# Performance work log

Hardware: AMD Instinct MI355X
Metric: run time of the kernel (lower is better)

The kernel has to match this reference:

```python
import jax, jax.numpy as jnp
import numpy as np

HIP_L, HIP_R = 11, 12          # hip joint indices along V
K_LIST = (2, 3, 4, 5)          # soft-selector kNN MoE k values
TAU = 0.35                     # tau_center for ball softmax
EPS = 1e-6


def _sym_norm(A):
    # D^{-1/2} A D^{-1/2} without materializing diag matrices
    d = A.sum(-1)
    dis = jax.lax.rsqrt(d + EPS)
    return dis[..., :, None] * A * dis[..., None, :]


def _knn_adj(pos, k):
    # pos: (N, M, 3) -> 0/1 kNN adjacency (+I self loop, diag ends up 2 as in torch ref)
    M = pos.shape[1]
    diff = pos[:, :, None, :] - pos[:, None, :, :]
    d = jnp.sqrt(jnp.sum(diff * diff, axis=-1))  # (N, M, M) euclidean cdist
    idx = jax.lax.top_k(-d, k)[1]                # (N, M, k) k smallest distances (incl. self)
    A = jax.nn.one_hot(idx, M, dtype=pos.dtype).sum(2)  # scatter 1.0 at kNN columns
    return A + jnp.eye(M, dtype=pos.dtype)


def setup_inputs() -> dict:
    key = jax.random.key(0)
    k1, k2 = jax.random.split(key)
    N, C, T, V, M = 64, 8, 300, 17, 12
    x = jax.random.normal(k1, (N, C, T, V, M), jnp.float32)
    alpha_logits = jax.random.normal(k2, (len(K_LIST),), jnp.float32) * 0.1
    lambda_fuse = jnp.array([0.1], jnp.float32)
    tag_gate = jnp.array([1.0], jnp.float32)
    return {"x": x, "alpha_logits": alpha_logits,
            "lambda_fuse": lambda_fuse, "tag_gate": tag_gate}


def reference(x, alpha_logits, lambda_fuse, tag_gate):
    N, C, T, V, M = x.shape
    # hip-root position averaged over time: (N, M, 3)
    root3 = 0.5 * (x[:, 0:3, :, HIP_L, :] + x[:, 0:3, :, HIP_R, :])  # (N,3,T,M)
    pos = root3.mean(2).transpose(0, 2, 1)                           # (N,M,3)

    # kNN mixture-of-graphs, sym-normalized, detached (detach_adj=True)
    A_knn_stack = jnp.stack([_sym_norm(_knn_adj(pos, k)) for k in K_LIST], 1)  # (N,K,M,M)
    A_knn_stack = jax.lax.stop_gradient(A_knn_stack)
    alpha = jax.nn.softmax(alpha_logits)          # global selector, temp=1
    A_knn = jnp.einsum('k,nkij->nij', alpha, A_knn_stack)

    # soft ball-star graph
    s = x[:, 3].mean((1, 2))                      # (N,M) ball score
    p = jax.nn.softmax(s / TAU, axis=1)
    A_ball = p[:, :, None] + p[:, None, :] + jnp.eye(M, dtype=x.dtype)
    A_ball = jax.lax.stop_gradient(_sym_norm(A_ball))

    # adaptive ball weight from confidence of p (NOT detached)
    w = jnp.clip((jnp.max(p, 1, keepdims=True) - 1.0 / M) / (1.0 - 1.0 / M + EPS), 0.0, 1.0)
    A = w[:, :, None] * A_ball + (1.0 - w[:, :, None]) * A_knn  # (N,M,M)

    # message passing across persons on hip-root features, fused back residually
    root = 0.5 * (x[:, :, :, HIP_L, :] + x[:, :, :, HIP_R, :])  # (N,C,T,M)
    agg = jnp.einsum('nuv,nctv->nctu', A, root)                 # (N,C,T,M)
    g = jnp.tanh(tag_gate[0])  # ramp=1 (ramp_epochs=0), gate_max=1
    return x + g * lambda_fuse[0] * (agg - root)[:, :, :, None, :]
```

## Files before the change

kernel.cpp:

```cpp
#include <hip/hip_runtime.h>
#include <math.h>

#define N_ 64
#define C_ 8
#define T_ 300
#define V_ 17
#define M_ 12
#define EPSF 1e-6f
#define TAUF 0.35f


__global__ __launch_bounds__(256) void k_reduce(const float* __restrict__ x,
                                                float* __restrict__ ws_pos,
                                                float* __restrict__ ws_s) {
    const int n = blockIdx.x;
    const int tid = threadIdx.x;
    __shared__ float pos_acc[36];
    __shared__ float s_acc[12];
    if (tid < 36) pos_acc[tid] = 0.f;
    if (tid < 12) s_acc[tid] = 0.f;
    __syncthreads();

    {
        float a[3][3];
        #pragma unroll
        for (int d = 0; d < 3; ++d)
            #pragma unroll
            for (int ph = 0; ph < 3; ++ph) a[d][ph] = 0.f;
        for (int e = tid; e < 3600; e += 768) {
            #pragma unroll
            for (int ph = 0; ph < 3; ++ph) {
                int ee = e + ph * 256;
                if (ee < 3600) {
                    int t = ee / 12, m = ee % 12;
                    #pragma unroll
                    for (int d = 0; d < 3; ++d) {
                        const float* xb = x + ((size_t)(n * C_ + d) * T_ + t) * (V_ * M_);
                        a[d][ph] += xb[132 + m] + xb[144 + m];
                    }
                }
            }
        }
        int m0 = tid % 12;
        #pragma unroll
        for (int ph = 0; ph < 3; ++ph) {
            int m = (m0 + 4 * ph) % 12;
            #pragma unroll
            for (int d = 0; d < 3; ++d) atomicAdd(&pos_acc[d * 12 + m], a[d][ph]);
        }
    }

    {
        float a0 = 0.f, a1 = 0.f, a2 = 0.f;
        const float* xs = x + (size_t)(n * C_ + 3) * T_ * V_ * M_;
        for (int e = tid; e < 61200; e += 768) {
            a0 += xs[e];
            if (e + 256 < 61200) a1 += xs[e + 256];
            if (e + 512 < 61200) a2 += xs[e + 512];
        }
        int m0 = tid % 12;
        atomicAdd(&s_acc[m0], a0);
        atomicAdd(&s_acc[(m0 + 4) % 12], a1);
        atomicAdd(&s_acc[(m0 + 8) % 12], a2);
    }
    __syncthreads();
    if (tid < 36) ws_pos[n * 36 + tid] = pos_acc[tid] * (0.5f / (float)T_);
    if (tid < 12) ws_s[n * 12 + tid] = s_acc[tid] * (1.f / (float)(T_ * V_));
}

__global__ __launch_bounds__(64) void k_adj(const float* __restrict__ ws_pos,
                                            const float* __restrict__ ws_s,
                                            const float* __restrict__ alpha_logits,
                                            float* __restrict__ ws_A) {
    const int n = blockIdx.x;
    const int tid = threadIdx.x;
    __shared__ float posx[12], posy[12], posz[12];
    __shared__ float dist[144];
    __shared__ int ord[60];
    __shared__ float p_s[12];
    __shared__ float alpha_s[4];
    __shared__ float w_s;

    if (tid < 12) {
        posx[tid] = ws_pos[n * 36 + 0 * 12 + tid];
        posy[tid] = ws_pos[n * 36 + 1 * 12 + tid];
        posz[tid] = ws_pos[n * 36 + 2 * 12 + tid];
    }
    if (tid == 0) {
        float l0 = alpha_logits[0], l1 = alpha_logits[1], l2 = alpha_logits[2], l3 = alpha_logits[3];
        float mx = fmaxf(fmaxf(l0, l1), fmaxf(l2, l3));
        float e0 = expf(l0 - mx), e1 = expf(l1 - mx), e2 = expf(l2 - mx), e3 = expf(l3 - mx);
        float s = e0 + e1 + e2 + e3;
        alpha_s[0] = e0 / s; alpha_s[1] = e1 / s; alpha_s[2] = e2 / s; alpha_s[3] = e3 / s;
    }
    if (tid == 1) {
        float sv[12];
        float mx = -1e30f;
        #pragma unroll
        for (int m = 0; m < 12; ++m) { sv[m] = ws_s[n * 12 + m] * (1.f / TAUF); mx = fmaxf(mx, sv[m]); }
        float sum = 0.f;
        #pragma unroll
        for (int m = 0; m < 12; ++m) { sv[m] = expf(sv[m] - mx); sum += sv[m]; }
        float maxp = 0.f;
        #pragma unroll
        for (int m = 0; m < 12; ++m) { sv[m] = sv[m] / sum; p_s[m] = sv[m]; maxp = fmaxf(maxp, sv[m]); }
        float w = (maxp - 1.f / 12.f) / (1.f - 1.f / 12.f + EPSF);
        w_s = fminf(fmaxf(w, 0.f), 1.f);
    }
    __syncthreads();

    for (int e = tid; e < 144; e += 64) {
        int i = e / 12, j = e % 12;
        float dx = posx[i] - posx[j], dy = posy[i] - posy[j], dz = posz[i] - posz[j];
        dist[e] = sqrtf(dx * dx + dy * dy + dz * dz);
    }
    __syncthreads();

    if (tid < 12) {
        int i = tid, mask = 0;
        #pragma unroll
        for (int r = 0; r < 5; ++r) {
            float bd = 1e30f; int bj = -1;
            #pragma unroll
            for (int j = 0; j < 12; ++j) {
                if (!((mask >> j) & 1)) {
                    float dd = dist[i * 12 + j];
                    if (dd < bd) { bd = dd; bj = j; }
                }
            }
            ord[i * 5 + r] = bj; mask |= (1 << bj);
        }
    }
    __syncthreads();

    float w = w_s;
    for (int e = tid; e < 144; e += 64) {
        int i = e / 12, j = e % 12;
        int rank = 5;
        #pragma unroll
        for (int r = 4; r >= 0; --r) if (ord[i * 5 + r] == j) rank = r;
        float diag = (i == j) ? 1.f : 0.f;
        float aknn = 0.f;
        #pragma unroll
        for (int kk = 0; kk < 4; ++kk) {
            int K = kk + 2;
            float val = ((rank < K) ? 1.f : 0.f) + diag;
            aknn += alpha_s[kk] * val / ((float)(K + 1) + EPSF);
        }
        float pi = p_s[i], pj = p_s[j];
        float di = 12.f * pi + 2.f, dj = 12.f * pj + 2.f;
        float ab = (pi + pj + diag) * rsqrtf(di + EPSF) * rsqrtf(dj + EPSF);
        ws_A[n * 144 + e] = w * ab + (1.f - w) * aknn;
    }
}

#define RT 30
__global__ __launch_bounds__(256) void k_main(const float* __restrict__ x,
                                              const float* __restrict__ ws_A,
                                              const float* __restrict__ lambda_fuse,
                                              const float* __restrict__ tag_gate,
                                              float* __restrict__ out) {
    const int n = blockIdx.y;
    const int r0 = blockIdx.x * RT;
    const int tid = threadIdx.x;
    __shared__ float Ash[144];
    __shared__ float root_sh[RT * 12];
    __shared__ float delta_sh[RT * 12];

    if (tid < 144) Ash[tid] = ws_A[n * 144 + tid];
    float scale = tanhf(tag_gate[0]) * lambda_fuse[0];

    const float* xn = x + (size_t)n * 2400 * 204;
    float* on = out + (size_t)n * 2400 * 204;

    for (int e = tid; e < RT * 12; e += 256) {
        int r = e / 12, v = e % 12;
        const float* row = xn + (size_t)(r0 + r) * 204;
        root_sh[e] = 0.5f * (row[132 + v] + row[144 + v]);
    }
    __syncthreads();
    for (int e = tid; e < RT * 12; e += 256) {
        int r = e / 12, u = e % 12;
        float acc = 0.f;
        #pragma unroll
        for (int v = 0; v < 12; ++v) acc += Ash[u * 12 + v] * root_sh[r * 12 + v];
        delta_sh[e] = scale * (acc - root_sh[e]);
    }
    __syncthreads();

    const float4* x4 = (const float4*)(xn + (size_t)r0 * 204);
    float4* o4 = (float4*)(on + (size_t)r0 * 204);
    for (int f = tid; f < RT * 51; f += 256) {
        int r = f / 51, j = f % 51;
        int m0 = (4 * j) % 12;
        float4 v = x4[(size_t)r * 51 + j];
        const float* d = &delta_sh[r * 12 + m0];
        v.x += d[0]; v.y += d[1]; v.z += d[2]; v.w += d[3];
        o4[(size_t)r * 51 + j] = v;
    }
}

extern "C" void kernel_launch(void* const* d_in, const int* in_sizes, int n_in,
                              void* d_out, int out_size, void* d_ws, size_t ws_size,
                              hipStream_t stream) {
    const float* x = (const float*)d_in[0];
    const float* alpha_logits = (const float*)d_in[1];
    const float* lambda_fuse = (const float*)d_in[2];
    const float* tag_gate = (const float*)d_in[3];
    float* out = (float*)d_out;

    float* ws = (float*)d_ws;
    float* ws_pos = ws;
    float* ws_s = ws + 64 * 36;
    float* ws_A = ws + 64 * 36 + 64 * 12;

    k_reduce<<<dim3(N_), dim3(256), 0, stream>>>(x, ws_pos, ws_s);
    k_adj<<<dim3(N_), dim3(64), 0, stream>>>(ws_pos, ws_s, alpha_logits, ws_A);
    k_main<<<dim3(2400 / RT, N_), dim3(256), 0, stream>>>(x, ws_A, lambda_fuse, tag_gate, out);
}
```

Before: 306.9 us.

## Split reduction kernel across time chunks with global atomics

The per-sample reduction kernel is split along the time axis into 10 chunks, so 640 blocks run instead of 64. Partial sums are combined with global atomicAdd into a workspace that is zeroed by a memset, and the scaling moves into the adjacency kernel. The hip-joint gather is also rewritten as a flat loop with per-element shared atomics. This targets low occupancy in the reduction, in exchange for an extra memset launch, global atomics, and non-deterministic summation order.

```diff
diff --git a/kernel.cpp b/kernel.cpp
--- a/kernel.cpp
+++ b/kernel.cpp
@@ -10,10 +10,14 @@
 #define TAUF 0.35f
 
 
+#define TSPLIT 10
+#define TCH (T_ / TSPLIT)
+
 __global__ __launch_bounds__(256) void k_reduce(const float* __restrict__ x,
                                                 float* __restrict__ ws_pos,
                                                 float* __restrict__ ws_s) {
     const int n = blockIdx.x;
+    const int t0 = blockIdx.y * TCH;
     const int tid = threadIdx.x;
     __shared__ float pos_acc[36];
     __shared__ float s_acc[12];
@@ -22,50 +26,30 @@
     __syncthreads();
 
     {
-        float a[3][3];
-        #pragma unroll
-        for (int d = 0; d < 3; ++d)
-            #pragma unroll
-            for (int ph = 0; ph < 3; ++ph) a[d][ph] = 0.f;
-        for (int e = tid; e < 3600; e += 768) {
-            #pragma unroll
-            for (int ph = 0; ph < 3; ++ph) {
-                int ee = e + ph * 256;
-                if (ee < 3600) {
-                    int t = ee / 12, m = ee % 12;
-                    #pragma unroll
-                    for (int d = 0; d < 3; ++d) {
-                        const float* xb = x + ((size_t)(n * C_ + d) * T_ + t) * (V_ * M_);
-                        a[d][ph] += xb[132 + m] + xb[144 + m];
-                    }
-                }
-            }
-        }
-        int m0 = tid % 12;
-        #pragma unroll
-        for (int ph = 0; ph < 3; ++ph) {
-            int m = (m0 + 4 * ph) % 12;
-            #pragma unroll
-            for (int d = 0; d < 3; ++d) atomicAdd(&pos_acc[d * 12 + m], a[d][ph]);
-        }
-    }
-
-    {
+        const float* xs = x + ((size_t)(n * C_ + 3) * T_ + t0) * 204;
         float a0 = 0.f, a1 = 0.f, a2 = 0.f;
-        const float* xs = x + (size_t)(n * C_ + 3) * T_ * V_ * M_;
-        for (int e = tid; e < 61200; e += 768) {
+        for (int e = tid; e < TCH * 204; e += 768) {
             a0 += xs[e];
-            if (e + 256 < 61200) a1 += xs[e + 256];
-            if (e + 512 < 61200) a2 += xs[e + 512];
+            if (e + 256 < TCH * 204) a1 += xs[e + 256];
+            if (e + 512 < TCH * 204) a2 += xs[e + 512];
         }
         int m0 = tid % 12;
         atomicAdd(&s_acc[m0], a0);
         atomicAdd(&s_acc[(m0 + 4) % 12], a1);
         atomicAdd(&s_acc[(m0 + 8) % 12], a2);
     }
-    __syncthreads();
-    if (tid < 36) ws_pos[n * 36 + tid] = pos_acc[tid] * (0.5f / (float)T_);
-    if (tid < 12) ws_s[n * 12 + tid] = s_acc[tid] * (1.f / (float)(T_ * V_));
+
+    for (int e = tid; e < 3 * TCH * 24; e += 256) {
+        int d = e / (TCH * 24);
+        int rem = e % (TCH * 24);
+        int tt = rem / 24, j = rem % 24;
+        float val = x[((size_t)(n * C_ + d) * T_ + t0 + tt) * 204 + 132 + j];
+        atomicAdd(&pos_acc[d * 12 + (j % 12)], val);
+    }
+    __syncthreads();
+
+    if (tid < 36) atomicAdd(&ws_pos[n * 36 + tid], pos_acc[tid]);
+    if (tid < 12) atomicAdd(&ws_s[n * 12 + tid], s_acc[tid]);
 }
 
 __global__ __launch_bounds__(64) void k_adj(const float* __restrict__ ws_pos,
@@ -81,10 +65,11 @@
     __shared__ float alpha_s[4];
     __shared__ float w_s;
 
+    const float PSC = 0.5f / (float)T_;
     if (tid < 12) {
-        posx[tid] = ws_pos[n * 36 + 0 * 12 + tid];
-        posy[tid] = ws_pos[n * 36 + 1 * 12 + tid];
-        posz[tid] = ws_pos[n * 36 + 2 * 12 + tid];
+        posx[tid] = ws_pos[n * 36 + 0 * 12 + tid] * PSC;
+        posy[tid] = ws_pos[n * 36 + 1 * 12 + tid] * PSC;
+        posz[tid] = ws_pos[n * 36 + 2 * 12 + tid] * PSC;
     }
     if (tid == 0) {
         float l0 = alpha_logits[0], l1 = alpha_logits[1], l2 = alpha_logits[2], l3 = alpha_logits[3];
@@ -94,10 +79,11 @@
         alpha_s[0] = e0 / s; alpha_s[1] = e1 / s; alpha_s[2] = e2 / s; alpha_s[3] = e3 / s;
     }
     if (tid == 1) {
+        const float SSC = 1.f / (float)(T_ * V_);
         float sv[12];
         float mx = -1e30f;
         #pragma unroll
-        for (int m = 0; m < 12; ++m) { sv[m] = ws_s[n * 12 + m] * (1.f / TAUF); mx = fmaxf(mx, sv[m]); }
+        for (int m = 0; m < 12; ++m) { sv[m] = (ws_s[n * 12 + m] * SSC) * (1.f / TAUF); mx = fmaxf(mx, sv[m]); }
         float sum = 0.f;
         #pragma unroll
         for (int m = 0; m < 12; ++m) { sv[m] = expf(sv[m] - mx); sum += sv[m]; }
@@ -212,9 +198,11 @@
     float* ws = (float*)d_ws;
     float* ws_pos = ws;
     float* ws_s = ws + 64 * 36;
-    float* ws_A = ws + 64 * 36 + 64 * 12;
-
-    k_reduce<<<dim3(N_), dim3(256), 0, stream>>>(x, ws_pos, ws_s);
+    float* ws_A = ws + 64 * 48;
+
+    hipMemsetAsync(ws, 0, (size_t)(64 * 48) * sizeof(float), stream);
+
+    k_reduce<<<dim3(N_, TSPLIT), dim3(256), 0, stream>>>(x, ws_pos, ws_s);
     k_adj<<<dim3(N_), dim3(64), 0, stream>>>(ws_pos, ws_s, alpha_logits, ws_A);
     k_main<<<dim3(2400 / RT, N_), dim3(256), 0, stream>>>(x, ws_A, lambda_fuse, tag_gate, out);
 }
```

Measured after the change: 255.6 us. 1.2x faster.
